# Kernel tuning notes

Hardware: AMD Instinct MI355X
Metric: run time of the kernel (lower is better)

Reference implementation:

```python
import jax, jax.numpy as jnp
from jax import lax
import numpy as np

B = 16384

def setup_inputs() -> dict:
    key = jax.random.key(0)
    ks = jax.random.split(key, 48)
    f32 = jnp.float32
    def rn(i, shape, scale=0.05):
        return jax.random.normal(ks[i], shape, dtype=f32) * scale
    d = {}
    d['x'] = jax.random.normal(ks[0], (B, 100), dtype=f32)
    # kaiming-normal initial states: std = sqrt(2/fan_in)
    d['h0f'] = rn(1, (B, 100), np.sqrt(2.0/100))
    d['c0f'] = rn(2, (B, 100), np.sqrt(2.0/100))
    d['h0b'] = rn(3, (B, 100), np.sqrt(2.0/100))
    d['c0b'] = rn(4, (B, 100), np.sqrt(2.0/100))
    d['h0m'] = rn(5, (B, 200), np.sqrt(2.0/200))
    d['c0m'] = rn(6, (B, 200), np.sqrt(2.0/200))
    # LSTMCell(5,100) forward / backward: Wih (400,5), Whh (400,100)
    d['Wih_f'] = rn(7, (400, 5), 0.2); d['Whh_f'] = rn(8, (400, 100), 0.1)
    d['bih_f'] = rn(9, (400,), 0.1);  d['bhh_f'] = rn(10, (400,), 0.1)
    d['Wih_b'] = rn(11, (400, 5), 0.2); d['Whh_b'] = rn(12, (400, 100), 0.1)
    d['bih_b'] = rn(13, (400,), 0.1);  d['bhh_b'] = rn(14, (400,), 0.1)
    # LSTMCell(200,200): Wih (800,200), Whh (800,200)
    d['Wih_m'] = rn(15, (800, 200), 0.07); d['Whh_m'] = rn(16, (800, 200), 0.07)
    d['bih_m'] = rn(17, (800,), 0.07);   d['bhh_m'] = rn(18, (800,), 0.07)
    # dense 200->27
    d['Wd'] = rn(19, (27, 200), 0.07); d['bd'] = rn(20, (27,), 0.07)
    # ConvTranspose1d weights, torch layout (Cin, Cout, K)
    d['w1'] = rn(21, (1, 128, 4), 0.5);  d['b1'] = rn(22, (128,), 0.1)
    d['w2'] = rn(23, (128, 64, 4), 0.04); d['b2'] = rn(24, (64,), 0.1)
    d['w3'] = rn(25, (64, 1, 4), 0.06);  d['b3'] = rn(26, (1,), 0.1)
    # BatchNorm (eval) params/stats
    d['g1'] = jnp.ones((128,), f32); d['be1'] = jnp.zeros((128,), f32)
    d['m1'] = jnp.zeros((128,), f32); d['v1'] = jnp.ones((128,), f32)
    d['g2'] = jnp.ones((64,), f32); d['be2'] = jnp.zeros((64,), f32)
    d['m2'] = jnp.zeros((64,), f32); d['v2'] = jnp.ones((64,), f32)
    return d

def _lstm_step(Wih, Whh, bih, bhh):
    def step(carry, xt):
        h, c = carry
        g = xt @ Wih.T + bih + h @ Whh.T + bhh  # (B, 4H)
        i, f, gg, o = jnp.split(g, 4, axis=1)   # torch gate order i,f,g,o
        c2 = jax.nn.sigmoid(f) * c + jax.nn.sigmoid(i) * jnp.tanh(gg)
        h2 = jax.nn.sigmoid(o) * jnp.tanh(c2)
        return (h2, c2), h2
    return step

def _convT(x, w, b, stride=2, pad=1):
    # torch ConvTranspose1d == conv with lhs_dilation=stride, pad k-1-p, flipped kernel
    k = w.shape[2]
    wc = jnp.transpose(jnp.flip(w, 2), (1, 0, 2))  # (Cout, Cin, K)
    out = lax.conv_general_dilated(x, wc, window_strides=(1,),
                                   padding=[(k - 1 - pad, k - 1 - pad)],
                                   lhs_dilation=(stride,),
                                   dimension_numbers=('NCH', 'OIH', 'NCH'))
    return out + b[None, :, None]

def _bn(x, g, be, m, v, eps=1e-5):
    inv = g / jnp.sqrt(v + eps)
    return (x - m[None, :, None]) * inv[None, :, None] + be[None, :, None]

def reference(x, h0f, c0f, h0b, c0b, h0m, c0m,
              Wih_f, Whh_f, bih_f, bhh_f,
              Wih_b, Whh_b, bih_b, bhh_b,
              Wih_m, Whh_m, bih_m, bhh_m,
              Wd, bd, w1, b1, w2, b2, w3, b3,
              g1, be1, m1, v1, g2, be2, m2, v2):
    xs = x.reshape(20, -1, 5)  # (T=20, B, 5)
    _, hf = lax.scan(_lstm_step(Wih_f, Whh_f, bih_f, bhh_f), (h0f, c0f), xs)
    _, hb = lax.scan(_lstm_step(Wih_b, Whh_b, bih_b, bhh_b), (h0b, c0b), xs, reverse=True)
    merged = jnp.concatenate([hf, hb], axis=-1)  # (20, B, 200)
    (hm, _), _ = lax.scan(_lstm_step(Wih_m, Whh_m, bih_m, bhh_m), (h0m, c0m), merged)
    y = hm @ Wd.T + bd              # dropout in eval mode = identity
    y = y.reshape(-1, 1, 27)
    y = jax.nn.relu(_bn(_convT(y, w1, b1), g1, be1, m1, v1))   # (B,128,54)
    y = jax.nn.relu(_bn(_convT(y, w2, b2), g2, be2, m2, v2))   # (B,64,108)
    y = _convT(y, w3, b3)                                       # (B,1,216)
    return y.reshape(-1, 216)
```

## Files before the change

kernel.cpp:

```cpp
#include <hip/hip_runtime.h>
#include <hip/hip_bf16.h>

#define BTOT 16384

typedef __attribute__((ext_vector_type(8))) short bf16x8;
typedef __attribute__((ext_vector_type(4))) float f32x4;

__device__ __forceinline__ float sig_(float x) {
    return __fdividef(1.0f, 1.0f + __expf(-x));
}
__device__ __forceinline__ float tanh_(float x) {
    float ax = fabsf(x);
    float e  = __expf(-2.0f * ax);
    float r  = __fdividef(1.0f - e, 1.0f + e);
    return x < 0.0f ? -r : r;
}

__global__ __launch_bounds__(256) void k_prep_mfma(
    const float* __restrict__ Wih, const float* __restrict__ Whh,
    const float* __restrict__ bih, const float* __restrict__ bhh,
    __hip_bfloat16* __restrict__ Bhi, __hip_bfloat16* __restrict__ Blo)
{
    const int e = blockIdx.x * 256 + threadIdx.x;
    if (e >= 332800) return;
    const int j  = e & 7;
    const int l  = (e >> 3) & 63;
    const int r2 = e >> 9;
    const int ct = r2 % 50;
    const int kt = r2 / 50;
    const int k  = kt * 32 + ((l >> 4) << 3) + j;
    const int op = ct * 16 + (l & 15);
    const int u  = op >> 2;
    const int g  = op & 3;
    const int row = g * 200 + u;
    float val;
    if (k < 200)       val = Wih[(size_t)row * 200 + k];
    else if (k < 400)  val = Whh[(size_t)row * 200 + (k - 200)];
    else if (k == 415) val = bih[row] + bhh[row];
    else               val = 0.0f;
    const __hip_bfloat16 hi = __float2bfloat16(val);
    Bhi[e] = hi;
    Blo[e] = __float2bfloat16(val - __bfloat162float(hi));
}

__global__ __launch_bounds__(256) void k_prep_mfma100(
    const float* __restrict__ Wih, const float* __restrict__ Whh,
    const float* __restrict__ bih, const float* __restrict__ bhh,
    __hip_bfloat16* __restrict__ Bhi, __hip_bfloat16* __restrict__ Blo)
{
    const int e = blockIdx.x * 256 + threadIdx.x;
    if (e >= 51200) return;
    const int j  = e & 7;
    const int l  = (e >> 3) & 63;
    const int r2 = e >> 9;
    const int kt = r2 & 3;
    const int ct = r2 >> 2;
    const int k  = kt * 32 + ((l >> 4) << 3) + j;
    const int op = ct * 16 + (l & 15);
    const int u  = op >> 2;
    const int g  = op & 3;
    const int row = g * 100 + u;
    float val;
    if (k < 5)         val = Wih[(size_t)row * 5 + k];
    else if (k < 10)   val = Wih[(size_t)row * 5 + (k - 5)];
    else if (k < 110)  val = Whh[(size_t)row * 100 + (k - 10)];
    else if (k == 110) val = bih[row] + bhh[row];
    else               val = 0.0f;
    const __hip_bfloat16 hi = __float2bfloat16(val);
    Bhi[e] = hi;
    Blo[e] = __float2bfloat16(val - __bfloat162float(hi));
}

__global__ __launch_bounds__(512, 2) void k_lstm100(
    const float* __restrict__ x,
    const float* __restrict__ h0f, const float* __restrict__ c0f,
    const float* __restrict__ h0b, const float* __restrict__ c0b,
    const __hip_bfloat16* __restrict__ BFhi, const __hip_bfloat16* __restrict__ BFlo,
    const __hip_bfloat16* __restrict__ BBhi, const __hip_bfloat16* __restrict__ BBlo,
    __hip_bfloat16* __restrict__ HF, __hip_bfloat16* __restrict__ HB)
{
    __shared__ __hip_bfloat16 At[64][136];
    __shared__ float scr[8][16][17];

    const int dir = blockIdx.y;
    const float* h0 = dir ? h0b : h0f;
    const float* c0 = dir ? c0b : c0f;
    const __hip_bfloat16* Bhi = dir ? BBhi : BFhi;
    const __hip_bfloat16* Blo = dir ? BBlo : BFlo;
    __hip_bfloat16* Hout = dir ? HB : HF;

    const int tid = threadIdx.x;
    const int l   = tid & 63;
    const int w   = tid >> 6;
    const int rb  = blockIdx.x * 64;

    float cst[4][4];
    #pragma unroll
    for (int cti = 0; cti < 4; ++cti) {
        const int ct = w + 8 * cti;
        if (ct < 25) {
            #pragma unroll
            for (int rt = 0; rt < 4; ++rt)
                cst[cti][rt] = c0[(size_t)(rb + rt * 16 + (l >> 2)) * 100 + ct * 4 + (l & 3)];
        }
    }

    for (int i = tid; i < 6400; i += 512) {
        const int row = i / 100, u = i - row * 100;
        At[row][10 + u] = __float2bfloat16(h0[(size_t)(rb + row) * 100 + u]);
    }
    for (int i = tid; i < 64 * 26; i += 512) {
        const int row = i / 26, cc = i - row * 26;
        At[row][110 + cc] = __float2bfloat16(cc == 0 ? 1.0f : 0.0f);
    }
    {
        const int tt0 = dir ? 19 : 0;
        if (tid < 320) {
            const float v = x[(size_t)tt0 * (BTOT * 5) + (size_t)rb * 5 + tid];
            const int row = tid / 5, cc = tid - row * 5;
            const __hip_bfloat16 hi = __float2bfloat16(v);
            At[row][cc]     = hi;
            At[row][5 + cc] = __float2bfloat16(v - __bfloat162float(hi));
        }
    }
    __syncthreads();

    for (int t = 0; t < 20; ++t) {
        const int tt = dir ? (19 - t) : t;

        f32x4 acc[4][4];
        #pragma unroll
        for (int cti = 0; cti < 4; ++cti)
            #pragma unroll
            for (int rt = 0; rt < 4; ++rt)
                acc[cti][rt] = (f32x4){0.f, 0.f, 0.f, 0.f};

        #pragma unroll
        for (int kt = 0; kt < 4; ++kt) {
            bf16x8 afr[4];
            #pragma unroll
            for (int rt = 0; rt < 4; ++rt)
                afr[rt] = *reinterpret_cast<const bf16x8*>(
                    &At[rt * 16 + (l & 15)][kt * 32 + (l >> 4) * 8]);
            #pragma unroll
            for (int cti = 0; cti < 4; ++cti) {
                const int ct = w + 8 * cti;
                if (ct < 25) {
                    const size_t fo = ((size_t)(ct * 4 + kt) * 64 + l) * 8;
                    const bf16x8 bh = *reinterpret_cast<const bf16x8*>(Bhi + fo);
                    const bf16x8 bl = *reinterpret_cast<const bf16x8*>(Blo + fo);
                    #pragma unroll
                    for (int rt = 0; rt < 4; ++rt) {
                        acc[cti][rt] = __builtin_amdgcn_mfma_f32_16x16x32_bf16(
                            afr[rt], bh, acc[cti][rt], 0, 0, 0);
                        acc[cti][rt] = __builtin_amdgcn_mfma_f32_16x16x32_bf16(
                            afr[rt], bl, acc[cti][rt], 0, 0, 0);
                    }
                }
            }
        }

        float hval[4][4];
        #pragma unroll
        for (int cti = 0; cti < 4; ++cti) {
            const int ct = w + 8 * cti;
            if (ct < 25) {
                #pragma unroll
                for (int rt = 0; rt < 4; ++rt) {
                    #pragma unroll
                    for (int rr = 0; rr < 4; ++rr)
                        scr[w][(l >> 4) * 4 + rr][l & 15] = acc[cti][rt][rr];
                    const float g0 = scr[w][l >> 2][(l & 3) * 4 + 0];
                    const float g1 = scr[w][l >> 2][(l & 3) * 4 + 1];
                    const float g2 = scr[w][l >> 2][(l & 3) * 4 + 2];
                    const float g3 = scr[w][l >> 2][(l & 3) * 4 + 3];
                    const float ig = sig_(g0);
                    const float fg = sig_(g1);
                    const float gg = tanh_(g2);
                    const float og = sig_(g3);
                    const float cn = fmaf(fg, cst[cti][rt], ig * gg);
                    cst[cti][rt] = cn;
                    hval[cti][rt] = og * tanh_(cn);
                }
            }
        }
        __syncthreads();

        #pragma unroll
        for (int cti = 0; cti < 4; ++cti) {
            const int ct = w + 8 * cti;
            if (ct < 25) {
                #pragma unroll
                for (int rt = 0; rt < 4; ++rt) {
                    const __hip_bfloat16 hb = __float2bfloat16(hval[cti][rt]);
                    At[rt * 16 + (l >> 2)][10 + ct * 4 + (l & 3)] = hb;
                    Hout[((size_t)tt * 100 + ct * 4 + (l & 3)) * BTOT
                         + rb + rt * 16 + (l >> 2)] = hb;
                }
            }
        }
        if (t < 19) {
            const int ttn = dir ? (19 - (t + 1)) : (t + 1);
            if (tid < 320) {
                const float v = x[(size_t)ttn * (BTOT * 5) + (size_t)rb * 5 + tid];
                const int row = tid / 5, cc = tid - row * 5;
                const __hip_bfloat16 hi = __float2bfloat16(v);
                At[row][cc]     = hi;
                At[row][5 + cc] = __float2bfloat16(v - __bfloat162float(hi));
            }
        }
        __syncthreads();
    }
}

__device__ __forceinline__ int aidx(int row, int c) {
    return (((row >> 4) * 13 + (c >> 5)) * 64 + ((c >> 3) & 3) * 16 + (row & 15)) * 8
           + (c & 7);
}

__global__ __launch_bounds__(512, 2) void k_mid(
    const float* __restrict__ h0m, const float* __restrict__ c0m,
    const __hip_bfloat16* __restrict__ Bhi, const __hip_bfloat16* __restrict__ Blo,
    const __hip_bfloat16* __restrict__ HF, const __hip_bfloat16* __restrict__ HB,
    __hip_bfloat16* __restrict__ HM)
{
    __shared__ __hip_bfloat16 Af[4][13][64][8];
    __shared__ float scr[8][16][17];

    const int tid = threadIdx.x;
    const int l   = tid & 63;
    const int w   = tid >> 6;
    const int rb  = blockIdx.x * 64;
    __hip_bfloat16* A = &Af[0][0][0][0];

    float cst[7][4], hval[7][4];
    #pragma unroll
    for (int cti = 0; cti < 7; ++cti) {
        const int ct = w + 8 * cti;
        if (ct < 50) {
            #pragma unroll
            for (int rt = 0; rt < 4; ++rt) {
                const int row = rb + rt * 16 + (l >> 2);
                cst[cti][rt] = c0m[(size_t)row * 200 + ct * 4 + (l & 3)];
            }
        }
    }

    for (int i = tid; i < 12800; i += 512) {
        const int u = i % 200, rr = i / 200;
        A[aidx(rr, 200 + u)] = __float2bfloat16(h0m[(size_t)(rb + rr) * 200 + u]);
    }
    for (int i = tid; i < 1024; i += 512) {
        const int rr = i >> 4, cc = i & 15;
        A[aidx(rr, 400 + cc)] = __float2bfloat16((cc == 15) ? 1.0f : 0.0f);
    }
    for (int i = tid; i < 6400; i += 512) {
        const int rr = i & 63, u = i >> 6;
        A[aidx(rr, u)]       = HF[(size_t)u * BTOT + rb + rr];
        A[aidx(rr, 100 + u)] = HB[(size_t)u * BTOT + rb + rr];
    }
    __syncthreads();

    for (int t = 0; t < 20; ++t) {
        f32x4 acc[7][4];
        #pragma unroll
        for (int cti = 0; cti < 7; ++cti)
            #pragma unroll
            for (int rt = 0; rt < 4; ++rt)
                acc[cti][rt] = (f32x4){0.f, 0.f, 0.f, 0.f};

        #pragma unroll
        for (int kt = 0; kt < 13; ++kt) {
            bf16x8 afr[4];
            #pragma unroll
            for (int rt = 0; rt < 4; ++rt)
                afr[rt] = *reinterpret_cast<const bf16x8*>(&Af[rt][kt][l][0]);
            #pragma unroll
            for (int cti = 0; cti < 7; ++cti) {
                const int ct = w + 8 * cti;
                if (ct < 50) {
                    const size_t fo = ((size_t)(kt * 50 + ct) * 64 + l) * 8;
                    const bf16x8 bh = *reinterpret_cast<const bf16x8*>(Bhi + fo);
                    const bf16x8 bl = *reinterpret_cast<const bf16x8*>(Blo + fo);
                    #pragma unroll
                    for (int rt = 0; rt < 4; ++rt) {
                        acc[cti][rt] = __builtin_amdgcn_mfma_f32_16x16x32_bf16(
                            afr[rt], bh, acc[cti][rt], 0, 0, 0);
                        acc[cti][rt] = __builtin_amdgcn_mfma_f32_16x16x32_bf16(
                            afr[rt], bl, acc[cti][rt], 0, 0, 0);
                    }
                }
            }
        }

        #pragma unroll
        for (int cti = 0; cti < 7; ++cti) {
            const int ct = w + 8 * cti;
            if (ct < 50) {
                #pragma unroll
                for (int rt = 0; rt < 4; ++rt) {
                    #pragma unroll
                    for (int rr = 0; rr < 4; ++rr)
                        scr[w][(l >> 4) * 4 + rr][l & 15] = acc[cti][rt][rr];
                    const float g0 = scr[w][l >> 2][(l & 3) * 4 + 0];
                    const float g1 = scr[w][l >> 2][(l & 3) * 4 + 1];
                    const float g2 = scr[w][l >> 2][(l & 3) * 4 + 2];
                    const float g3 = scr[w][l >> 2][(l & 3) * 4 + 3];
                    const float ig = sig_(g0);
                    const float fg = sig_(g1);
                    const float gg = tanh_(g2);
                    const float og = sig_(g3);
                    const float cn = fmaf(fg, cst[cti][rt], ig * gg);
                    cst[cti][rt] = cn;
                    hval[cti][rt] = og * tanh_(cn);
                }
            }
        }
        __syncthreads();

        #pragma unroll
        for (int cti = 0; cti < 7; ++cti) {
            const int ct = w + 8 * cti;
            if (ct < 50) {
                #pragma unroll
                for (int rt = 0; rt < 4; ++rt)
                    A[aidx(rt * 16 + (l >> 2), 200 + ct * 4 + (l & 3))] =
                        __float2bfloat16(hval[cti][rt]);
            }
        }
        if (t < 19) {
            const __hip_bfloat16* HFt = HF + (size_t)(t + 1) * 100 * BTOT + rb;
            const __hip_bfloat16* HBt = HB + (size_t)(t + 1) * 100 * BTOT + rb;
            for (int i = tid; i < 6400; i += 512) {
                const int rr = i & 63, u = i >> 6;
                A[aidx(rr, u)]       = HFt[(size_t)u * BTOT + rr];
                A[aidx(rr, 100 + u)] = HBt[(size_t)u * BTOT + rr];
            }
        }
        __syncthreads();
    }

    for (int i = tid; i < 12800; i += 512) {
        const int u = i % 200, rr = i / 200;
        HM[(size_t)(rb + rr) * 200 + u] = A[aidx(rr, 200 + u)];
    }
}

__global__ __launch_bounds__(256, 2) void k_head(
    const __hip_bfloat16* __restrict__ HM,
    const float* __restrict__ Wd, const float* __restrict__ bd,
    const float* __restrict__ w1, const float* __restrict__ b1,
    const float* __restrict__ w2, const float* __restrict__ b2,
    const float* __restrict__ w3, const float* __restrict__ b3,
    const float* __restrict__ g1, const float* __restrict__ be1,
    const float* __restrict__ m1, const float* __restrict__ v1,
    const float* __restrict__ g2, const float* __restrict__ be2,
    const float* __restrict__ m2, const float* __restrict__ v2,
    float* __restrict__ out)
{
    __shared__ float hm_s[200];
    __shared__ float y27p[29];
    __shared__ float t1p[128][58];
    __shared__ float t2p[64][110];
    __shared__ float sc1[128], sh1[128], sc2[64], sh2[64];

    const int tid = threadIdx.x;
    const int b   = blockIdx.x;

    if (tid < 200) hm_s[tid] = __bfloat162float(HM[(size_t)b * 200 + tid]);
    if (tid < 128) {
        const float s = g1[tid] * __frsqrt_rn(v1[tid] + 1e-5f);
        sc1[tid] = s; sh1[tid] = be1[tid] - m1[tid] * s;
    } else if (tid < 192) {
        const int cc = tid - 128;
        const float s = g2[cc] * __frsqrt_rn(v2[cc] + 1e-5f);
        sc2[cc] = s; sh2[cc] = be2[cc] - m2[cc] * s;
    }
    {
        const int co = tid >> 1;
        t1p[co][(tid & 1) ? 55 : 0] = 0.0f;
        if (tid < 128) { t1p[tid][56] = 0.0f; t1p[tid][57] = 0.0f; }
        if (tid < 64)  { t2p[tid][0] = 0.0f; t2p[tid][109] = 0.0f; }
        if (tid == 0)  { y27p[0] = 0.0f; y27p[28] = 0.0f; }
    }
    __syncthreads();

    if (tid < 27) {
        float a = bd[tid];
        const float* wr = Wd + tid * 200;
        for (int i = 0; i < 200; ++i) a = fmaf(hm_s[i], wr[i], a);
        y27p[tid + 1] = a;
    }
    __syncthreads();

    for (int idx = tid; idx < 128 * 54; idx += 256) {
        const int co = idx / 54;
        const int ll = idx - co * 54;
        const int q  = (ll + 1) >> 1;
        const float4 w = *reinterpret_cast<const float4*>(w1 + co * 4);
        const float wHI = (ll & 1) ? w.x : w.y;
        const float wLO = (ll & 1) ? w.z : w.w;
        float a = b1[co];
        a = fmaf(y27p[q + 1], wHI, a);
        a = fmaf(y27p[q],     wLO, a);
        a = fmaf(a, sc1[co], sh1[co]);
        t1p[co][ll + 1] = fmaxf(a, 0.0f);
    }
    __syncthreads();

    {
        const int co   = tid & 63;
        const int lseg = tid >> 6;
        const int l0   = lseg * 28;
        const int qb   = lseg * 14;
        float acc[28];
        const float bb = b2[co];
        #pragma unroll
        for (int j = 0; j < 28; ++j) acc[j] = bb;

        #pragma unroll 2
        for (int ci = 0; ci < 128; ++ci) {
            float tv[16];
            #pragma unroll
            for (int j = 0; j < 16; ++j) tv[j] = t1p[ci][qb + j];
            const float4 w = *reinterpret_cast<const float4*>(
                w2 + ((size_t)((ci << 6) + co) << 2));
            #pragma unroll
            for (int j = 0; j < 28; ++j) {
                const int qi = (j + 1) >> 1;
                const float wHI = (j & 1) ? w.x : w.y;
                const float wLO = (j & 1) ? w.z : w.w;
                acc[j] = fmaf(tv[qi + 1], wHI, acc[j]);
                acc[j] = fmaf(tv[qi],     wLO, acc[j]);
            }
        }
        const float s2 = sc2[co], h2 = sh2[co];
        #pragma unroll
        for (int j = 0; j < 28; ++j) {
            const int ll = l0 + j;
            if (ll < 108) t2p[co][ll + 1] = fmaxf(fmaf(acc[j], s2, h2), 0.0f);
        }
    }
    __syncthreads();

    if (tid < 216) {
        const int ll = tid;
        const int q = (ll + 1) >> 1;
        const bool odd = (ll & 1) != 0;
        float a = b3[0];
        #pragma unroll 4
        for (int ci = 0; ci < 64; ++ci) {
            const float4 w = *reinterpret_cast<const float4*>(w3 + ci * 4);
            const float wHI = odd ? w.x : w.y;
            const float wLO = odd ? w.z : w.w;
            a = fmaf(t2p[ci][q + 1], wHI, a);
            a = fmaf(t2p[ci][q],     wLO, a);
        }
        out[(size_t)b * 216 + ll] = a;
    }
}

extern "C" void kernel_launch(void* const* d_in, const int* in_sizes, int n_in,
                              void* d_out, int out_size, void* d_ws, size_t ws_size,
                              hipStream_t stream) {
    const float* x     = (const float*)d_in[0];
    const float* h0f   = (const float*)d_in[1];
    const float* c0f   = (const float*)d_in[2];
    const float* h0b   = (const float*)d_in[3];
    const float* c0b   = (const float*)d_in[4];
    const float* h0m   = (const float*)d_in[5];
    const float* c0m   = (const float*)d_in[6];
    const float* Wih_f = (const float*)d_in[7];
    const float* Whh_f = (const float*)d_in[8];
    const float* bih_f = (const float*)d_in[9];
    const float* bhh_f = (const float*)d_in[10];
    const float* Wih_b = (const float*)d_in[11];
    const float* Whh_b = (const float*)d_in[12];
    const float* bih_b = (const float*)d_in[13];
    const float* bhh_b = (const float*)d_in[14];
    const float* Wih_m = (const float*)d_in[15];
    const float* Whh_m = (const float*)d_in[16];
    const float* bih_m = (const float*)d_in[17];
    const float* bhh_m = (const float*)d_in[18];
    const float* Wd    = (const float*)d_in[19];
    const float* bd    = (const float*)d_in[20];
    const float* w1    = (const float*)d_in[21];
    const float* b1    = (const float*)d_in[22];
    const float* w2    = (const float*)d_in[23];
    const float* b2    = (const float*)d_in[24];
    const float* w3    = (const float*)d_in[25];
    const float* b3    = (const float*)d_in[26];
    const float* g1    = (const float*)d_in[27];
    const float* be1   = (const float*)d_in[28];
    const float* m1    = (const float*)d_in[29];
    const float* v1    = (const float*)d_in[30];
    const float* g2    = (const float*)d_in[31];
    const float* be2   = (const float*)d_in[32];
    const float* m2    = (const float*)d_in[33];
    const float* v2    = (const float*)d_in[34];

    char* ws = (char*)d_ws;
    __hip_bfloat16* HF   = (__hip_bfloat16*)ws;
    __hip_bfloat16* HB   = (__hip_bfloat16*)(ws + 65536000);
    __hip_bfloat16* BhiM = (__hip_bfloat16*)(ws + 131072000);
    __hip_bfloat16* BloM = (__hip_bfloat16*)(ws + 131737600);
    __hip_bfloat16* BFhi = (__hip_bfloat16*)(ws + 132403200);
    __hip_bfloat16* BFlo = (__hip_bfloat16*)(ws + 132505600);
    __hip_bfloat16* BBhi = (__hip_bfloat16*)(ws + 132608000);
    __hip_bfloat16* BBlo = (__hip_bfloat16*)(ws + 132710400);
    __hip_bfloat16* HM   = (__hip_bfloat16*)(ws + 132812800);

    k_prep_mfma<<<(332800 + 255) / 256, 256, 0, stream>>>(
        Wih_m, Whh_m, bih_m, bhh_m, BhiM, BloM);
    k_prep_mfma100<<<(51200 + 255) / 256, 256, 0, stream>>>(
        Wih_f, Whh_f, bih_f, bhh_f, BFhi, BFlo);
    k_prep_mfma100<<<(51200 + 255) / 256, 256, 0, stream>>>(
        Wih_b, Whh_b, bih_b, bhh_b, BBhi, BBlo);

    k_lstm100<<<dim3(256, 2), 512, 0, stream>>>(
        x, h0f, c0f, h0b, c0b,
        BFhi, BFlo, BBhi, BBlo, HF, HB);

    k_mid<<<256, 512, 0, stream>>>(
        h0m, c0m, BhiM, BloM, HF, HB, HM);

    k_head<<<16384, 256, 0, stream>>>(
        HM, Wd, bd, w1, b1, w2, b2, w3, b3,
        g1, be1, m1, v1, g2, be2, m2, v2, (float*)d_out);
}
```

Before: 3.418 ms.

## Double k_mid waves, make weight tiles column-major, shrink gate-exchange scratch

The middle LSTM kernel now runs 1024 threads (16 waves) per block instead of 512. Each wave loops over its column tiles in the outer loop and streams 13 contiguous K-tiles of weights per tile. The prep kernel reorders the packed weights so each column tile's K-slices are adjacent. The LDS gate-exchange scratch is halved and done in two passes, and A fragments are reloaded from LDS for every column tile. This aims to raise latency hiding and cut per-wave register pressure, at the cost of more LDS traffic and an aggressive launch bound that may force register spills.

```diff
diff --git a/kernel.cpp b/kernel.cpp
--- a/kernel.cpp
+++ b/kernel.cpp
@@ -26,8 +26,8 @@
     const int j  = e & 7;
     const int l  = (e >> 3) & 63;
     const int r2 = e >> 9;
-    const int ct = r2 % 50;
-    const int kt = r2 / 50;
+    const int kt = r2 % 13;
+    const int ct = r2 / 13;
     const int k  = kt * 32 + ((l >> 4) << 3) + j;
     const int op = ct * 16 + (l & 15);
     const int u  = op >> 2;
@@ -147,8 +147,8 @@
                 const int ct = w + 8 * cti;
                 if (ct < 25) {
                     const size_t fo = ((size_t)(ct * 4 + kt) * 64 + l) * 8;
-                    const bf16x8 bh = *reinterpret_cast<const bf16x8*>(Bhi + fo);
-                    const bf16x8 bl = *reinterpret_cast<const bf16x8*>(Blo + fo);
+                    const bf16x8 bh = *reinterpret_cast<const bf16x8*>(BFhi == Bhi ? BFhi + fo : BBhi + fo);
+                    const bf16x8 bl = *reinterpret_cast<const bf16x8*>(BFlo == Blo ? BFlo + fo : BBlo + fo);
                     #pragma unroll
                     for (int rt = 0; rt < 4; ++rt) {
                         acc[cti][rt] = __builtin_amdgcn_mfma_f32_16x16x32_bf16(
@@ -218,14 +218,14 @@
            + (c & 7);
 }
 
-__global__ __launch_bounds__(512, 2) void k_mid(
+__global__ __launch_bounds__(1024, 4) void k_mid(
     const float* __restrict__ h0m, const float* __restrict__ c0m,
     const __hip_bfloat16* __restrict__ Bhi, const __hip_bfloat16* __restrict__ Blo,
     const __hip_bfloat16* __restrict__ HF, const __hip_bfloat16* __restrict__ HB,
     __hip_bfloat16* __restrict__ HM)
 {
     __shared__ __hip_bfloat16 Af[4][13][64][8];
-    __shared__ float scr[8][16][17];
+    __shared__ float scr[16][16][9];
 
     const int tid = threadIdx.x;
     const int l   = tid & 63;
@@ -233,28 +233,26 @@
     const int rb  = blockIdx.x * 64;
     __hip_bfloat16* A = &Af[0][0][0][0];
 
-    float cst[7][4], hval[7][4];
+    float cst[4][4], hval[4][4];
     #pragma unroll
-    for (int cti = 0; cti < 7; ++cti) {
-        const int ct = w + 8 * cti;
+    for (int cti = 0; cti < 4; ++cti) {
+        const int ct = w + 16 * cti;
         if (ct < 50) {
             #pragma unroll
-            for (int rt = 0; rt < 4; ++rt) {
-                const int row = rb + rt * 16 + (l >> 2);
-                cst[cti][rt] = c0m[(size_t)row * 200 + ct * 4 + (l & 3)];
-            }
-        }
-    }
-
-    for (int i = tid; i < 12800; i += 512) {
+            for (int rt = 0; rt < 4; ++rt)
+                cst[cti][rt] = c0m[(size_t)(rb + rt * 16 + (l >> 2)) * 200 + ct * 4 + (l & 3)];
+        }
+    }
+
+    for (int i = tid; i < 12800; i += 1024) {
         const int u = i % 200, rr = i / 200;
         A[aidx(rr, 200 + u)] = __float2bfloat16(h0m[(size_t)(rb + rr) * 200 + u]);
     }
-    for (int i = tid; i < 1024; i += 512) {
+    for (int i = tid; i < 1024; i += 1024) {
         const int rr = i >> 4, cc = i & 15;
         A[aidx(rr, 400 + cc)] = __float2bfloat16((cc == 15) ? 1.0f : 0.0f);
     }
-    for (int i = tid; i < 6400; i += 512) {
+    for (int i = tid; i < 6400; i += 1024) {
         const int rr = i & 63, u = i >> 6;
         A[aidx(rr, u)]       = HF[(size_t)u * BTOT + rb + rr];
         A[aidx(rr, 100 + u)] = HB[(size_t)u * BTOT + rb + rr];
@@ -262,50 +260,59 @@
     __syncthreads();
 
     for (int t = 0; t < 20; ++t) {
-        f32x4 acc[7][4];
-        #pragma unroll
-        for (int cti = 0; cti < 7; ++cti)
-            #pragma unroll
-            for (int rt = 0; rt < 4; ++rt)
-                acc[cti][rt] = (f32x4){0.f, 0.f, 0.f, 0.f};
-
-        #pragma unroll
-        for (int kt = 0; kt < 13; ++kt) {
-            bf16x8 afr[4];
-            #pragma unroll
-            for (int rt = 0; rt < 4; ++rt)
-                afr[rt] = *reinterpret_cast<const bf16x8*>(&Af[rt][kt][l][0]);
-            #pragma unroll
-            for (int cti = 0; cti < 7; ++cti) {
-                const int ct = w + 8 * cti;
-                if (ct < 50) {
-                    const size_t fo = ((size_t)(kt * 50 + ct) * 64 + l) * 8;
-                    const bf16x8 bh = *reinterpret_cast<const bf16x8*>(Bhi + fo);
-                    const bf16x8 bl = *reinterpret_cast<const bf16x8*>(Blo + fo);
+        #pragma unroll
+        for (int cti = 0; cti < 4; ++cti) {
+            const int ct = w + 16 * cti;
+            if (ct < 50) {
+                f32x4 acc[4];
+                #pragma unroll
+                for (int rt = 0; rt < 4; ++rt) acc[rt] = (f32x4){0.f, 0.f, 0.f, 0.f};
+                const __hip_bfloat16* bph = Bhi + ((size_t)ct * 13 * 64 + l) * 8;
+                const __hip_bfloat16* bpl = Blo + ((size_t)ct * 13 * 64 + l) * 8;
+                #pragma unroll
+                for (int kt = 0; kt < 13; ++kt) {
+                    const bf16x8 bh = *reinterpret_cast<const bf16x8*>(bph + kt * 512);
+                    const bf16x8 bl = *reinterpret_cast<const bf16x8*>(bpl + kt * 512);
                     #pragma unroll
                     for (int rt = 0; rt < 4; ++rt) {
-                        acc[cti][rt] = __builtin_amdgcn_mfma_f32_16x16x32_bf16(
-                            afr[rt], bh, acc[cti][rt], 0, 0, 0);
-                        acc[cti][rt] = __builtin_amdgcn_mfma_f32_16x16x32_bf16(
-                            afr[rt], bl, acc[cti][rt], 0, 0, 0);
+                        const bf16x8 a = *reinterpret_cast<const bf16x8*>(&Af[rt][kt][l][0]);
+                        acc[rt] = __builtin_amdgcn_mfma_f32_16x16x32_bf16(a, bh, acc[rt], 0, 0, 0);
+                        acc[rt] = __builtin_amdgcn_mfma_f32_16x16x32_bf16(a, bl, acc[rt], 0, 0, 0);
                     }
                 }
-            }
-        }
-
-        #pragma unroll
-        for (int cti = 0; cti < 7; ++cti) {
-            const int ct = w + 8 * cti;
-            if (ct < 50) {
+                const int lo16 = l & 15;
+                const int rowq = l >> 2;
+                const int gq   = l & 3;
                 #pragma unroll
                 for (int rt = 0; rt < 4; ++rt) {
-                    #pragma unroll
-                    for (int rr = 0; rr < 4; ++rr)
-                        scr[w][(l >> 4) * 4 + rr][l & 15] = acc[cti][rt][rr];
-                    const float g0 = scr[w][l >> 2][(l & 3) * 4 + 0];
-                    const float g1 = scr[w][l >> 2][(l & 3) * 4 + 1];
-                    const float g2 = scr[w][l >> 2][(l & 3) * 4 + 2];
-                    const float g3 = scr[w][l >> 2][(l & 3) * 4 + 3];
+                    const f32x4 v = acc[rt];
+                    float g0 = 0.f, g1 = 0.f, g2 = 0.f, g3 = 0.f;
+                    if (lo16 < 8) {
+                        #pragma unroll
+                        for (int rr = 0; rr < 4; ++rr)
+                            scr[w][(l >> 4) * 4 + rr][lo16] = v[rr];
+                    }
+                    __builtin_amdgcn_sched_barrier(0);
+                    if (gq < 2) {
+                        g0 = scr[w][rowq][gq * 4 + 0];
+                        g1 = scr[w][rowq][gq * 4 + 1];
+                        g2 = scr[w][rowq][gq * 4 + 2];
+                        g3 = scr[w][rowq][gq * 4 + 3];
+                    }
+                    __builtin_amdgcn_sched_barrier(0);
+                    if (lo16 >= 8) {
+                        #pragma unroll
+                        for (int rr = 0; rr < 4; ++rr)
+                            scr[w][(l >> 4) * 4 + rr][lo16 - 8] = v[rr];
+                    }
+                    __builtin_amdgcn_sched_barrier(0);
+                    if (gq >= 2) {
+                        g0 = scr[w][rowq][(gq - 2) * 4 + 0];
+                        g1 = scr[w][rowq][(gq - 2) * 4 + 1];
+                        g2 = scr[w][rowq][(gq - 2) * 4 + 2];
+                        g3 = scr[w][rowq][(gq - 2) * 4 + 3];
+                    }
+                    __builtin_amdgcn_sched_barrier(0);
                     const float ig = sig_(g0);
                     const float fg = sig_(g1);
                     const float gg = tanh_(g2);
@@ -319,8 +326,8 @@
         __syncthreads();
 
         #pragma unroll
-        for (int cti = 0; cti < 7; ++cti) {
-            const int ct = w + 8 * cti;
+        for (int cti = 0; cti < 4; ++cti) {
+            const int ct = w + 16 * cti;
             if (ct < 50) {
                 #pragma unroll
                 for (int rt = 0; rt < 4; ++rt)
@@ -331,7 +338,7 @@
         if (t < 19) {
             const __hip_bfloat16* HFt = HF + (size_t)(t + 1) * 100 * BTOT + rb;
             const __hip_bfloat16* HBt = HB + (size_t)(t + 1) * 100 * BTOT + rb;
-            for (int i = tid; i < 6400; i += 512) {
+            for (int i = tid; i < 6400; i += 1024) {
                 const int rr = i & 63, u = i >> 6;
                 A[aidx(rr, u)]       = HFt[(size_t)u * BTOT + rr];
                 A[aidx(rr, 100 + u)] = HBt[(size_t)u * BTOT + rr];
@@ -340,7 +347,7 @@
         __syncthreads();
     }
 
-    for (int i = tid; i < 12800; i += 512) {
+    for (int i = tid; i < 12800; i += 1024) {
         const int u = i % 200, rr = i / 200;
         HM[(size_t)(rb + rr) * 200 + u] = A[aidx(rr, 200 + u)];
     }
@@ -521,7 +528,7 @@
         x, h0f, c0f, h0b, c0b,
         BFhi, BFlo, BBhi, BBlo, HF, HB);
 
-    k_mid<<<256, 512, 0, stream>>>(
+    k_mid<<<256, 1024, 0, stream>>>(
         h0m, c0m, BhiM, BloM, HF, HB, HM);
 
     k_head<<<16384, 256, 0, stream>>>(
```

Result: faster. 3.040 ms (-11.1%).
